# Kernel optimization log

Hardware: AMD Instinct MI355X
Metric: run time of the kernel (lower is better)

## Reference

```python
import jax, jax.numpy as jnp
import numpy as np
import math

D, H, FF, B, S = 512, 8, 2048, 2, 2048
DK = D // H


def _ln(x, g, b, eps=1e-5):
    m = jnp.mean(x, axis=-1, keepdims=True)
    v = jnp.var(x, axis=-1, keepdims=True)
    return (x - m) / jnp.sqrt(v + eps) * g + b


def _mha(q_in, kv_in, Wq, bq, Wk, bk, Wv, bv, Wo, bo):
    Bq, Sq, _ = q_in.shape
    Sk = kv_in.shape[1]
    q = (q_in @ Wq + bq).reshape(Bq, Sq, H, DK).transpose(0, 2, 1, 3)
    k = (kv_in @ Wk + bk).reshape(Bq, Sk, H, DK).transpose(0, 2, 1, 3)
    v = (kv_in @ Wv + bv).reshape(Bq, Sk, H, DK).transpose(0, 2, 1, 3)
    # NOTE: source uses float floor-division `//` by sqrt(dk); replicate faithfully.
    scores = jnp.floor(jnp.einsum('bhqd,bhkd->bhqk', q, k) / math.sqrt(DK))
    # NOTE: source calls scores.masked_fill(...) without assigning -> mask has no effect.
    attn = jax.nn.softmax(scores, axis=-1)
    out = jnp.einsum('bhqk,bhkd->bhqd', attn, v)
    out = out.transpose(0, 2, 1, 3).reshape(Bq, Sq, D)
    return out @ Wo + bo


def setup_inputs() -> dict:
    key = jax.random.key(0)
    ks = jax.random.split(key, 16)
    w = lambda k, shp: jax.random.normal(k, shp, jnp.float32) * 0.02
    inp = {
        'x': jax.random.normal(ks[0], (B, S, D), jnp.float32),
        'enc_out': jax.random.normal(ks[1], (B, S, D), jnp.float32),
        'src_mask': jnp.ones((B, 1, 1, S), jnp.int32),
        'tgt_mask': jnp.ones((B, 1, S, S), jnp.int32),
    }
    for i, pre in enumerate(['sa', 'ca']):
        kk = jax.random.split(ks[2 + i], 4)
        for j, nm in enumerate(['Wq', 'Wk', 'Wv', 'Wo']):
            inp[f'{pre}_{nm}'] = w(kk[j], (D, D))
            inp[f'{pre}_{nm[1].lower()}b'] = jnp.zeros((D,), jnp.float32)
    inp['ff_W1'] = w(ks[4], (D, FF)); inp['ff_b1'] = jnp.zeros((FF,), jnp.float32)
    inp['ff_W2'] = w(ks[5], (FF, D)); inp['ff_b2'] = jnp.zeros((D,), jnp.float32)
    for i in range(3):
        inp[f'ln{i}_g'] = jnp.ones((D,), jnp.float32)
        inp[f'ln{i}_b'] = jnp.zeros((D,), jnp.float32)
    return inp


def reference(x, enc_out, src_mask, tgt_mask,
              sa_Wq, sa_qb, sa_Wk, sa_kb, sa_Wv, sa_vb, sa_Wo, sa_ob,
              ca_Wq, ca_qb, ca_Wk, ca_kb, ca_Wv, ca_vb, ca_Wo, ca_ob,
              ff_W1, ff_b1, ff_W2, ff_b2,
              ln0_g, ln0_b, ln1_g, ln1_b, ln2_g, ln2_b):
    x = _ln(x + _mha(x, x, sa_Wq, sa_qb, sa_Wk, sa_kb, sa_Wv, sa_vb, sa_Wo, sa_ob), ln0_g, ln0_b)
    x = _ln(x + _mha(x, enc_out, ca_Wq, ca_qb, ca_Wk, ca_kb, ca_Wv, ca_vb, ca_Wo, ca_ob), ln1_g, ln1_b)
    ff = jax.nn.relu(x @ ff_W1 + ff_b1) @ ff_W2 + ff_b2
    x = _ln(x + ff, ln2_g, ln2_b)
    return x
```

## Files before the change

### kernel.cpp

```cpp
#include <hip/hip_runtime.h>
#include <math.h>


typedef __attribute__((ext_vector_type(8))) short short8;
typedef __attribute__((ext_vector_type(4))) float f32x4;

#define MFMA16(a, b, c) __builtin_amdgcn_mfma_f32_16x16x32_bf16((a), (b), (c), 0, 0, 0)

__device__ __forceinline__ unsigned short f2bf(float f) {
    unsigned int u = __float_as_uint(f);
    u += 0x7fffu + ((u >> 16) & 1u);
    return (unsigned short)(u >> 16);
}
__device__ __forceinline__ float bf2f(unsigned short h) {
    return __uint_as_float(((unsigned int)h) << 16);
}
__device__ __forceinline__ void g2l16(const void* g, void* l) {
    __builtin_amdgcn_global_load_lds(
        (const __attribute__((address_space(1))) unsigned int*)g,
        (__attribute__((address_space(3))) unsigned int*)l, 16, 0, 0);
}
__device__ __forceinline__ int swz(int row, int col) {
    return row * 64 + (col ^ ((row & 7) * 8));
}
__device__ __forceinline__ void xcd_remap(int& bx, int& by, int& bz) {
    const int gx = gridDim.x, gy = gridDim.y;
    const int nwg = gx * gy * gridDim.z;
    const int flat = blockIdx.x + gx * (blockIdx.y + gy * blockIdx.z);
    const int s = (flat & 7) * (nwg >> 3) + (flat >> 3);
    bx = s % gx; const int t = s / gx; by = t % gy; bz = t / gy;
}

template <int BM, int BN, int MODE>
__global__ __launch_bounds__(256, (BM == 64) ? 4 : (BN == 128 ? 2 : 3))
void gemm_bf16(
    const unsigned short* __restrict__ A, const unsigned short* __restrict__ Bt,
    const float* __restrict__ bias, float* __restrict__ Cf,
    unsigned short* __restrict__ O1,
    int M, int N, int K)
{
    __shared__ unsigned short As[2][BM * 64];
    __shared__ unsigned short Bs[2][BN * 64];
    const int tid = threadIdx.x, wv = tid >> 6, lane = tid & 63;
    const int l15 = lane & 15, l4 = lane >> 4;
    int bx, by, bz; xcd_remap(bx, by, bz);
    const int bm = by * BM, bn = bx * BN;
    constexpr int MI = (BM == 64) ? 1 : (BN == 128 ? 4 : 2);
    constexpr int AJ = (BM == 64) ? 2 : 4;
    constexpr int BJ = (BN == 128) ? 4 : 2;
    const int wrow = (BM == 64) ? wv * 16 : (BN == 128 ? (wv >> 1) * 64 : wv * 32);
    const int wcol = (BN == 128) ? (wv & 1) * 64 : 0;
    const int aw = (BM == 64) ? wv * 16 : wv * 32;
    const int bw = (BN == 128) ? wv * 32 : wv * 16;

    f32x4 acc[MI][4];
    #pragma unroll
    for (int i = 0; i < MI; ++i)
        #pragma unroll
        for (int j = 0; j < 4; ++j) acc[i][j] = (f32x4){0.f, 0.f, 0.f, 0.f};

    const int srow = lane >> 3;
    const int sch  = (lane & 7) ^ srow;
    const unsigned short* Asrc = A + (size_t)(bm + aw + srow) * K + sch * 8;
    const unsigned short* Bsrc = Bt + (size_t)(bn + bw + srow) * K + sch * 8;

    auto stage = [&](int buf, int k0) {
        #pragma unroll
        for (int j = 0; j < AJ; ++j)
            g2l16(Asrc + (size_t)j * 8 * K + k0, &As[buf][(aw + j * 8) * 64]);
        #pragma unroll
        for (int j = 0; j < BJ; ++j)
            g2l16(Bsrc + (size_t)j * 8 * K + k0, &Bs[buf][(bw + j * 8) * 64]);
    };

    stage(0, 0);
    __syncthreads();
    int cur = 0;
    for (int k0 = 0; k0 < K; k0 += 64) {
        if (k0 + 64 < K) stage(cur ^ 1, k0 + 64);
        #pragma unroll
        for (int kk = 0; kk < 2; ++kk) {
            const int kc = kk * 32 + l4 * 8;
            short8 af[MI], bfr[4];
            #pragma unroll
            for (int mi = 0; mi < MI; ++mi)
                af[mi] = *(const short8*)&As[cur][swz(wrow + mi * 16 + l15, kc)];
            #pragma unroll
            for (int nf = 0; nf < 4; ++nf)
                bfr[nf] = *(const short8*)&Bs[cur][swz(wcol + nf * 16 + l15, kc)];
            __builtin_amdgcn_s_setprio(1);
            #pragma unroll
            for (int mi = 0; mi < MI; ++mi)
                #pragma unroll
                for (int nf = 0; nf < 4; ++nf)
                    acc[mi][nf] = MFMA16(af[mi], bfr[nf], acc[mi][nf]);
            __builtin_amdgcn_s_setprio(0);
        }
        __syncthreads();
        cur ^= 1;
    }

    #pragma unroll
    for (int nf = 0; nf < 4; ++nf) {
        const int n = bn + wcol + nf * 16 + l15;
        const float bv = bias[n];
        #pragma unroll
        for (int mi = 0; mi < MI; ++mi) {
            const int m0 = bm + wrow + mi * 16 + l4 * 4;
            #pragma unroll
            for (int r = 0; r < 4; ++r) {
                float v = acc[mi][nf][r] + bv;
                size_t idx = (size_t)(m0 + r) * N + n;
                if (MODE == 0) Cf[idx] = v;
                else           O1[idx] = f2bf(fmaxf(v, 0.f));
            }
        }
    }
}

struct QKVArgs {
    const unsigned short* A[3];
    const unsigned short* Bt[3];
    const float* bias[3];
    unsigned short* O1[3];
    int mode[3];
};
__global__ __launch_bounds__(256, 3) void qkv_gemm(QKVArgs ja)
{
    __shared__ unsigned short As[2][128 * 64];
    __shared__ unsigned short Bs[2][64 * 64];
    const int tid = threadIdx.x, wv = tid >> 6, lane = tid & 63;
    const int l15 = lane & 15, l4 = lane >> 4;
    int bx, by, bz; xcd_remap(bx, by, bz);
    const int bm = by * 128, bn = bx * 64;
    const unsigned short* A  = ja.A[bz];
    const unsigned short* Bt = ja.Bt[bz];
    const int mode = ja.mode[bz];

    f32x4 acc[2][4];
    #pragma unroll
    for (int i = 0; i < 2; ++i)
        #pragma unroll
        for (int j = 0; j < 4; ++j) acc[i][j] = (f32x4){0.f, 0.f, 0.f, 0.f};

    const int srow = lane >> 3, sch = (lane & 7) ^ srow;
    const unsigned short* Asrc = A + (size_t)(bm + wv * 32 + srow) * 512 + sch * 8;
    const unsigned short* Bsrc = Bt + (size_t)(bn + wv * 16 + srow) * 512 + sch * 8;

    auto stage = [&](int buf, int k0) {
        #pragma unroll
        for (int j = 0; j < 4; ++j)
            g2l16(Asrc + (size_t)j * 8 * 512 + k0, &As[buf][(wv * 32 + j * 8) * 64]);
        #pragma unroll
        for (int j = 0; j < 2; ++j)
            g2l16(Bsrc + (size_t)j * 8 * 512 + k0, &Bs[buf][(wv * 16 + j * 8) * 64]);
    };

    stage(0, 0);
    __syncthreads();
    int cur = 0;
    for (int k0 = 0; k0 < 512; k0 += 64) {
        if (k0 + 64 < 512) stage(cur ^ 1, k0 + 64);
        #pragma unroll
        for (int kk = 0; kk < 2; ++kk) {
            const int kc = kk * 32 + l4 * 8;
            short8 af[2], bfr[4];
            af[0] = *(const short8*)&As[cur][swz(wv * 32 + l15, kc)];
            af[1] = *(const short8*)&As[cur][swz(wv * 32 + 16 + l15, kc)];
            #pragma unroll
            for (int nf = 0; nf < 4; ++nf)
                bfr[nf] = *(const short8*)&Bs[cur][swz(nf * 16 + l15, kc)];
            __builtin_amdgcn_s_setprio(1);
            #pragma unroll
            for (int mi = 0; mi < 2; ++mi)
                #pragma unroll
                for (int nf = 0; nf < 4; ++nf)
                    acc[mi][nf] = MFMA16(af[mi], bfr[nf], acc[mi][nf]);
            __builtin_amdgcn_s_setprio(0);
        }
        __syncthreads();
        cur ^= 1;
    }

    #pragma unroll
    for (int nf = 0; nf < 4; ++nf) {
        const int n = bn + nf * 16 + l15;
        const float bv = ja.bias[bz][n];
        #pragma unroll
        for (int mi = 0; mi < 2; ++mi) {
            const int m0 = bm + wv * 32 + mi * 16 + l4 * 4;
            if (mode == 2) {
                ushort4 pk;
                pk.x = f2bf(acc[mi][nf][0] + bv);
                pk.y = f2bf(acc[mi][nf][1] + bv);
                pk.z = f2bf(acc[mi][nf][2] + bv);
                pk.w = f2bf(acc[mi][nf][3] + bv);
                const int hh = n >> 6, dd = n & 63, bb = m0 >> 11, key = m0 & 2047;
                *(ushort4*)(ja.O1[bz] + ((((size_t)bb * 8 + hh) * 64 + dd) * 2048 + key)) = pk;
            } else {
                #pragma unroll
                for (int r = 0; r < 4; ++r)
                    ja.O1[bz][(size_t)(m0 + r) * 512 + n] = f2bf(acc[mi][nf][r] + bv);
            }
        }
    }
}

__global__ __launch_bounds__(256, 2) void attn_mfma(
    const unsigned short* __restrict__ Qb, const unsigned short* __restrict__ Kb,
    const unsigned short* __restrict__ Vt,
    float* __restrict__ PO0, float* __restrict__ PO1, float* __restrict__ PL)
{
    __shared__ unsigned short KH[2][64 * 64];
    __shared__ unsigned short VT[2][64 * 64];
    __shared__ unsigned short PS[64 * 64];

    const int tid = threadIdx.x, wv = tid >> 6, lane = tid & 63;
    const int l15 = lane & 15, l4 = lane >> 4;
    int bx, by, bz; xcd_remap(bx, by, bz);
    const int bh = by, b = bh >> 3, h = bh & 7;
    const int q0 = bx * 64;
    const int srow = lane >> 3;
    const int sch  = (lane & 7) ^ srow;
    const int kt0 = bz * 16, kt1 = kt0 + 16;

    short8 qh[2];
    {
        const size_t qrow = (size_t)(b * 2048 + q0 + wv * 16 + l15) * 512 + h * 64;
        qh[0] = *(const short8*)(Qb + qrow + l4 * 8);
        qh[1] = *(const short8*)(Qb + qrow + 32 + l4 * 8);
    }

    const unsigned short* k_src  = Kb + (size_t)(b * 2048 + wv * 16 + srow) * 512 + h * 64 + sch * 8;
    const unsigned short* vt_src = Vt + (size_t)(bh * 64 + wv * 16 + srow) * 2048 + sch * 8;

    auto stageKV = [&](int buf, int kt) {
        const size_t k0 = (size_t)kt * 64;
        #pragma unroll
        for (int j = 0; j < 2; ++j) {
            g2l16(k_src + (k0 + j * 8) * 512, &KH[buf][(wv * 16 + j * 8) * 64]);
            g2l16(vt_src + k0 + (size_t)j * 8 * 2048, &VT[buf][(wv * 16 + j * 8) * 64]);
        }
    };

    f32x4 o[4], lacc;
    #pragma unroll
    for (int i = 0; i < 4; ++i) o[i] = (f32x4){0.f, 0.f, 0.f, 0.f};
    lacc = (f32x4){0.f, 0.f, 0.f, 0.f};

    const short one_s = (short)(l15 == 0 ? 0x3F80 : 0);
    const short8 oneb = {one_s, one_s, one_s, one_s, one_s, one_s, one_s, one_s};

    stageKV(0, kt0);
    __syncthreads();
    int cur = 0;
    for (int kt = kt0; kt < kt1; ++kt) {
        if (kt + 1 < kt1) stageKV(cur ^ 1, kt + 1);

        f32x4 s[4];
        __builtin_amdgcn_s_setprio(1);
        #pragma unroll
        for (int f = 0; f < 4; ++f) {
            s[f] = (f32x4){0.f, 0.f, 0.f, 0.f};
            #pragma unroll
            for (int kk = 0; kk < 2; ++kk) {
                short8 kbf = *(const short8*)&KH[cur][swz(f * 16 + l15, kk * 32 + l4 * 8)];
                s[f] = MFMA16(qh[kk], kbf, s[f]);
            }
        }
        __builtin_amdgcn_s_setprio(0);

        #pragma unroll
        for (int f = 0; f < 4; ++f)
            #pragma unroll
            for (int r = 0; r < 4; ++r)
                PS[swz(wv * 16 + l4 * 4 + r, f * 16 + l15)] =
                    f2bf(__expf(floorf(s[f][r] * 0.125f)));

        short8 pa[2];
        pa[0] = *(const short8*)&PS[swz(wv * 16 + l15, l4 * 8)];
        pa[1] = *(const short8*)&PS[swz(wv * 16 + l15, 32 + l4 * 8)];

        __builtin_amdgcn_s_setprio(1);
        lacc = MFMA16(pa[0], oneb, lacc);
        lacc = MFMA16(pa[1], oneb, lacc);
        #pragma unroll
        for (int df = 0; df < 4; ++df) {
            #pragma unroll
            for (int kk = 0; kk < 2; ++kk) {
                short8 vb = *(const short8*)&VT[cur][swz(df * 16 + l15, kk * 32 + l4 * 8)];
                o[df] = MFMA16(pa[kk], vb, o[df]);
            }
        }
        __builtin_amdgcn_s_setprio(0);
        __syncthreads();
        cur ^= 1;
    }

    float* PO = bz ? PO1 : PO0;
    #pragma unroll
    for (int df = 0; df < 4; ++df)
        #pragma unroll
        for (int r = 0; r < 4; ++r)
            PO[(size_t)(b * 2048 + q0 + wv * 16 + l4 * 4 + r) * 512 + h * 64 + df * 16 + l15]
                = o[df][r];
    if (l15 == 0) {
        #pragma unroll
        for (int r = 0; r < 4; ++r)
            PL[(bz * 16 + bh) * 2048 + q0 + wv * 16 + l4 * 4 + r] = lacc[r];
    }
}

__global__ __launch_bounds__(256) void attn_combine(
    const float* __restrict__ po0, const float* __restrict__ po1,
    const float* __restrict__ pl, unsigned short* __restrict__ Ob)
{
    const size_t i = ((size_t)blockIdx.x * 256 + threadIdx.x) * 8;
    const int row = (int)(i >> 9), col = (int)(i & 511);
    const int b = row >> 11, q = row & 2047, h = col >> 6;
    const int bh = b * 8 + h;
    const float inv = 1.f / (pl[bh * 2048 + q] + pl[(16 + bh) * 2048 + q]);
    float4 a0 = *(const float4*)(po0 + i), a1 = *(const float4*)(po0 + i + 4);
    float4 c0 = *(const float4*)(po1 + i), c1 = *(const float4*)(po1 + i + 4);
    uint4 u;
    u.x = (unsigned)f2bf((a0.x + c0.x) * inv) | ((unsigned)f2bf((a0.y + c0.y) * inv) << 16);
    u.y = (unsigned)f2bf((a0.z + c0.z) * inv) | ((unsigned)f2bf((a0.w + c0.w) * inv) << 16);
    u.z = (unsigned)f2bf((a1.x + c1.x) * inv) | ((unsigned)f2bf((a1.y + c1.y) * inv) << 16);
    u.w = (unsigned)f2bf((a1.z + c1.z) * inv) | ((unsigned)f2bf((a1.w + c1.w) * inv) << 16);
    *(uint4*)(Ob + i) = u;
}

template <bool XBF, bool OUTF, bool OUTB>
__global__ __launch_bounds__(256) void add_ln(
    const void* __restrict__ Xv, const float* __restrict__ R,
    const float* __restrict__ g, const float* __restrict__ beta,
    float* __restrict__ OutF, unsigned short* __restrict__ OutB)
{
    const int row = blockIdx.x * 4 + (threadIdx.x >> 6);
    const int lane = threadIdx.x & 63;
    const int c0 = lane * 8;
    float v[8];
    const float* rr = R + (size_t)row * 512 + c0;
    float4 r0 = *(const float4*)rr, r1 = *(const float4*)(rr + 4);
    float xx[8];
    if (XBF) {
        const unsigned short* xr = (const unsigned short*)Xv + (size_t)row * 512 + c0;
        uint4 u = *(const uint4*)xr;
        xx[0] = bf2f(u.x & 0xffff); xx[1] = bf2f(u.x >> 16);
        xx[2] = bf2f(u.y & 0xffff); xx[3] = bf2f(u.y >> 16);
        xx[4] = bf2f(u.z & 0xffff); xx[5] = bf2f(u.z >> 16);
        xx[6] = bf2f(u.w & 0xffff); xx[7] = bf2f(u.w >> 16);
    } else {
        const float* xr = (const float*)Xv + (size_t)row * 512 + c0;
        float4 a0 = *(const float4*)xr, a1 = *(const float4*)(xr + 4);
        xx[0] = a0.x; xx[1] = a0.y; xx[2] = a0.z; xx[3] = a0.w;
        xx[4] = a1.x; xx[5] = a1.y; xx[6] = a1.z; xx[7] = a1.w;
    }
    v[0] = xx[0] + r0.x; v[1] = xx[1] + r0.y; v[2] = xx[2] + r0.z; v[3] = xx[3] + r0.w;
    v[4] = xx[4] + r1.x; v[5] = xx[5] + r1.y; v[6] = xx[6] + r1.z; v[7] = xx[7] + r1.w;
    float s = 0.f, s2 = 0.f;
    #pragma unroll
    for (int j = 0; j < 8; ++j) { s += v[j]; s2 += v[j] * v[j]; }
    #pragma unroll
    for (int off = 1; off < 64; off <<= 1) {
        s  += __shfl_xor(s, off);
        s2 += __shfl_xor(s2, off);
    }
    const float mean = s * (1.f / 512.f);
    const float var = s2 * (1.f / 512.f) - mean * mean;
    const float rs = 1.f / sqrtf(var + 1e-5f);
    float ovals[8];
    const float* gg = g + c0; const float* bb = beta + c0;
    #pragma unroll
    for (int j = 0; j < 8; ++j) ovals[j] = (v[j] - mean) * rs * gg[j] + bb[j];
    if (OUTF) {
        float* po = OutF + (size_t)row * 512 + c0;
        *(float4*)po = (float4){ovals[0], ovals[1], ovals[2], ovals[3]};
        *(float4*)(po + 4) = (float4){ovals[4], ovals[5], ovals[6], ovals[7]};
    }
    if (OUTB) {
        uint4 u;
        u.x = (unsigned)f2bf(ovals[0]) | ((unsigned)f2bf(ovals[1]) << 16);
        u.y = (unsigned)f2bf(ovals[2]) | ((unsigned)f2bf(ovals[3]) << 16);
        u.z = (unsigned)f2bf(ovals[4]) | ((unsigned)f2bf(ovals[5]) << 16);
        u.w = (unsigned)f2bf(ovals[6]) | ((unsigned)f2bf(ovals[7]) << 16);
        *(uint4*)(OutB + (size_t)row * 512 + c0) = u;
    }
}

struct WTJobs {
    const float* src[10];
    unsigned short* dst[10];
    int K[10], N[10];
    int cum[11];
};
__global__ __launch_bounds__(256) void prep(
    const float* __restrict__ X, const float* __restrict__ E,
    unsigned short* __restrict__ Xb, unsigned short* __restrict__ Eb, WTJobs jb)
{
    __shared__ float T[32][33];
    const int bid = blockIdx.x;
    if (bid < 2048) {
        size_t i = ((size_t)bid * 256 + threadIdx.x) * 8;
        const float* src; unsigned short* dst; size_t off;
        if (i < 2097152) { src = X; dst = Xb; off = i; }
        else             { src = E; dst = Eb; off = i - 2097152; }
        float4 a = *(const float4*)(src + off), c = *(const float4*)(src + off + 4);
        uint4 u;
        u.x = (unsigned)f2bf(a.x) | ((unsigned)f2bf(a.y) << 16);
        u.y = (unsigned)f2bf(a.z) | ((unsigned)f2bf(a.w) << 16);
        u.z = (unsigned)f2bf(c.x) | ((unsigned)f2bf(c.y) << 16);
        u.w = (unsigned)f2bf(c.z) | ((unsigned)f2bf(c.w) << 16);
        *(uint4*)(dst + off) = u;
        return;
    }
    int wb = bid - 2048;
    int z = 0;
    while (wb >= jb.cum[z + 1]) ++z;
    const int lt = wb - jb.cum[z];
    const int K = jb.K[z], N = jb.N[z];
    const int ntx = N >> 5;
    const int tx = lt % ntx, ty = lt / ntx;
    const int r = threadIdx.x >> 3, c4 = (threadIdx.x & 7) * 4;
    float4 a = *(const float4*)(jb.src[z] + (size_t)(ty * 32 + r) * N + tx * 32 + c4);
    T[r][c4] = a.x; T[r][c4 + 1] = a.y; T[r][c4 + 2] = a.z; T[r][c4 + 3] = a.w;
    __syncthreads();
    ushort4 o;
    o.x = f2bf(T[c4][r]); o.y = f2bf(T[c4 + 1][r]);
    o.z = f2bf(T[c4 + 2][r]); o.w = f2bf(T[c4 + 3][r]);
    *(ushort4*)(jb.dst[z] + (size_t)(tx * 32 + r) * K + ty * 32 + c4) = o;
}

extern "C" void kernel_launch(void* const* d_in, const int* in_sizes, int n_in,
                              void* d_out, int out_size, void* d_ws, size_t ws_size,
                              hipStream_t stream)
{
    const float* x   = (const float*)d_in[0];
    const float* enc = (const float*)d_in[1];
    const float* Wp[8] = {(const float*)d_in[4],  (const float*)d_in[6],
                          (const float*)d_in[8],  (const float*)d_in[10],
                          (const float*)d_in[12], (const float*)d_in[14],
                          (const float*)d_in[16], (const float*)d_in[18]};
    const float* sa_qb = (const float*)d_in[5],  *sa_kb = (const float*)d_in[7];
    const float* sa_vb = (const float*)d_in[9],  *sa_ob = (const float*)d_in[11];
    const float* ca_qb = (const float*)d_in[13], *ca_kb = (const float*)d_in[15];
    const float* ca_vb = (const float*)d_in[17], *ca_ob = (const float*)d_in[19];
    const float* ff_W1 = (const float*)d_in[20], *ff_b1 = (const float*)d_in[21];
    const float* ff_W2 = (const float*)d_in[22], *ff_b2 = (const float*)d_in[23];
    const float* ln0_g = (const float*)d_in[24], *ln0_b = (const float*)d_in[25];
    const float* ln1_g = (const float*)d_in[26], *ln1_b = (const float*)d_in[27];
    const float* ln2_g = (const float*)d_in[28], *ln2_b = (const float*)d_in[29];

    char* base = (char*)d_ws;
    const size_t MB = 1u << 20;
    unsigned short* wt   = (unsigned short*)(base + 0 * MB);
    unsigned short* xb   = (unsigned short*)(base + 8 * MB);
    unsigned short* encb = (unsigned short*)(base + 12 * MB);
    unsigned short* x1b  = (unsigned short*)(base + 16 * MB);
    unsigned short* attnb= (unsigned short*)(base + 20 * MB);
    unsigned short* vt   = (unsigned short*)(base + 24 * MB);
    unsigned short* qb   = (unsigned short*)(base + 28 * MB);
    unsigned short* kb   = (unsigned short*)(base + 32 * MB);
    unsigned short* ffb  = qb;
    unsigned short* x2b  = xb;
    float* proj = (float*)(base + 44 * MB);
    float* pl   = (float*)(base + 52 * MB);
    float* po0  = proj;
    float* po1  = (float*)d_out;
    float* out  = (float*)d_out;

    unsigned short* wtp[10];
    for (int i = 0; i < 8; ++i) wtp[i] = wt + (size_t)i * 262144;
    wtp[8] = wt + 8u * 262144;
    wtp[9] = wt + 8u * 262144 + 1048576;

    WTJobs jb;
    for (int i = 0; i < 8; ++i) { jb.src[i] = Wp[i]; jb.dst[i] = wtp[i]; jb.K[i] = 512; jb.N[i] = 512; }
    jb.src[8] = ff_W1; jb.dst[8] = wtp[8]; jb.K[8] = 512;  jb.N[8] = 2048;
    jb.src[9] = ff_W2; jb.dst[9] = wtp[9]; jb.K[9] = 2048; jb.N[9] = 512;
    jb.cum[0] = 0;
    for (int i = 0; i < 10; ++i)
        jb.cum[i + 1] = jb.cum[i] + (jb.N[i] >> 5) * (jb.K[i] >> 5);

    QKVArgs sa, ca;
    sa.A[0] = xb;  sa.Bt[0] = wtp[0]; sa.bias[0] = sa_qb; sa.O1[0] = qb; sa.mode[0] = 4;
    sa.A[1] = xb;  sa.Bt[1] = wtp[1]; sa.bias[1] = sa_kb; sa.O1[1] = kb; sa.mode[1] = 4;
    sa.A[2] = xb;  sa.Bt[2] = wtp[2]; sa.bias[2] = sa_vb; sa.O1[2] = vt; sa.mode[2] = 2;
    ca.A[0] = x1b;  ca.Bt[0] = wtp[4]; ca.bias[0] = ca_qb; ca.O1[0] = qb; ca.mode[0] = 4;
    ca.A[1] = encb; ca.Bt[1] = wtp[5]; ca.bias[1] = ca_kb; ca.O1[1] = kb; ca.mode[1] = 4;
    ca.A[2] = encb; ca.Bt[2] = wtp[6]; ca.bias[2] = ca_vb; ca.O1[2] = vt; ca.mode[2] = 2;

    dim3 blk(256);
    dim3 gqkv(8, 32, 3);
    dim3 g64(8, 64);
    dim3 gff1(16, 32);
    dim3 gattn(32, 16, 2);
    dim3 gln(1024);

    prep<<<2048 + jb.cum[10], blk, 0, stream>>>(x, enc, xb, encb, jb);

    qkv_gemm<<<gqkv, blk, 0, stream>>>(sa);
    attn_mfma<<<gattn, blk, 0, stream>>>(qb, kb, vt, po0, po1, pl);
    attn_combine<<<1024, blk, 0, stream>>>(po0, po1, pl, attnb);
    gemm_bf16<64, 64, 0><<<g64, blk, 0, stream>>>(attnb, wtp[3], sa_ob, proj, nullptr, 4096, 512, 512);
    add_ln<false, false, true><<<gln, blk, 0, stream>>>(x, proj, ln0_g, ln0_b, nullptr, x1b);

    qkv_gemm<<<gqkv, blk, 0, stream>>>(ca);
    attn_mfma<<<gattn, blk, 0, stream>>>(qb, kb, vt, po0, po1, pl);
    attn_combine<<<1024, blk, 0, stream>>>(po0, po1, pl, attnb);
    gemm_bf16<64, 64, 0><<<g64, blk, 0, stream>>>(attnb, wtp[7], ca_ob, proj, nullptr, 4096, 512, 512);
    add_ln<true, false, true><<<gln, blk, 0, stream>>>(x1b, proj, ln1_g, ln1_b, nullptr, x2b);

    gemm_bf16<128, 128, 3><<<gff1, blk, 0, stream>>>(x2b, wtp[8], ff_b1, nullptr, ffb, 4096, 2048, 512);
    gemm_bf16<64, 64, 0><<<g64, blk, 0, stream>>>(ffb, wtp[9], ff_b2, proj, nullptr, 4096, 512, 2048);
    add_ln<true, true, false><<<gln, blk, 0, stream>>>(x2b, proj, ln2_g, ln2_b, out, nullptr);
}
```

Before: 186.5 us.

## Store projection outputs in bf16 and permute P/V layout for packed stores

The output-projection and FF2 GEMMs now write bf16 instead of fp32, and add_ln gains a template flag to read a bf16 residual. This halves the traffic for the projection buffer on three write/read round-trips, at the cost of rounding the pre-LayerNorm residual to bf16. In attention, the P tile is now written with packed v_cvt_pk_bf16_f32 and 8-byte stores instead of scalar 2-byte stores. The V-transpose layout is permuted within 64-key blocks to match the new P column order. The V-transpose write in the QKV GEMM now uses strided scalar stores instead of a ushort4 store.

```diff
diff --git a/kernel.cpp b/kernel.cpp
--- a/kernel.cpp
+++ b/kernel.cpp
@@ -111,8 +111,9 @@
             for (int r = 0; r < 4; ++r) {
                 float v = acc[mi][nf][r] + bv;
                 size_t idx = (size_t)(m0 + r) * N + n;
-                if (MODE == 0) Cf[idx] = v;
-                else           O1[idx] = f2bf(fmaxf(v, 0.f));
+                if (MODE == 0)      Cf[idx] = v;
+                else if (MODE == 3) O1[idx] = f2bf(fmaxf(v, 0.f));
+                else                O1[idx] = f2bf(v);
             }
         }
     }
@@ -190,13 +191,14 @@
         for (int mi = 0; mi < 2; ++mi) {
             const int m0 = bm + wv * 32 + mi * 16 + l4 * 4;
             if (mode == 2) {
-                ushort4 pk;
-                pk.x = f2bf(acc[mi][nf][0] + bv);
-                pk.y = f2bf(acc[mi][nf][1] + bv);
-                pk.z = f2bf(acc[mi][nf][2] + bv);
-                pk.w = f2bf(acc[mi][nf][3] + bv);
-                const int hh = n >> 6, dd = n & 63, bb = m0 >> 11, key = m0 & 2047;
-                *(ushort4*)(ja.O1[bz] + ((((size_t)bb * 8 + hh) * 64 + dd) * 2048 + key)) = pk;
+                const int hh = n >> 6, dd = n & 63, bb = m0 >> 11;
+                const int key = m0 & 2047;
+                const int f = (key & 63) >> 4, j0 = key & 15;
+                const size_t basevt = (((size_t)bb * 8 + hh) * 64 + dd) * 2048
+                                    + (key & ~63) + f;
+                #pragma unroll
+                for (int r = 0; r < 4; ++r)
+                    ja.O1[bz][basevt + (size_t)(j0 + r) * 4] = f2bf(acc[mi][nf][r] + bv);
             } else {
                 #pragma unroll
                 for (int r = 0; r < 4; ++r)
@@ -271,11 +273,16 @@
         __builtin_amdgcn_s_setprio(0);
 
         #pragma unroll
-        for (int f = 0; f < 4; ++f)
-            #pragma unroll
-            for (int r = 0; r < 4; ++r)
-                PS[swz(wv * 16 + l4 * 4 + r, f * 16 + l15)] =
-                    f2bf(__expf(floorf(s[f][r] * 0.125f)));
+        for (int r = 0; r < 4; ++r) {
+            float p0 = __expf(floorf(s[0][r] * 0.125f));
+            float p1 = __expf(floorf(s[1][r] * 0.125f));
+            float p2 = __expf(floorf(s[2][r] * 0.125f));
+            float p3 = __expf(floorf(s[3][r] * 0.125f));
+            unsigned u0, u1;
+            asm("v_cvt_pk_bf16_f32 %0, %1, %2" : "=v"(u0) : "v"(p0), "v"(p1));
+            asm("v_cvt_pk_bf16_f32 %0, %1, %2" : "=v"(u1) : "v"(p2), "v"(p3));
+            *(uint2*)&PS[swz(wv * 16 + l4 * 4 + r, l15 * 4)] = (uint2){u0, u1};
+        }
 
         short8 pa[2];
         pa[0] = *(const short8*)&PS[swz(wv * 16 + l15, l4 * 8)];
@@ -330,19 +337,16 @@
     *(uint4*)(Ob + i) = u;
 }
 
-template <bool XBF, bool OUTF, bool OUTB>
+template <bool XBF, bool RBF, bool OUTF, bool OUTB>
 __global__ __launch_bounds__(256) void add_ln(
-    const void* __restrict__ Xv, const float* __restrict__ R,
+    const void* __restrict__ Xv, const void* __restrict__ Rv,
     const float* __restrict__ g, const float* __restrict__ beta,
     float* __restrict__ OutF, unsigned short* __restrict__ OutB)
 {
     const int row = blockIdx.x * 4 + (threadIdx.x >> 6);
     const int lane = threadIdx.x & 63;
     const int c0 = lane * 8;
-    float v[8];
-    const float* rr = R + (size_t)row * 512 + c0;
-    float4 r0 = *(const float4*)rr, r1 = *(const float4*)(rr + 4);
-    float xx[8];
+    float xx[8], rr[8], v[8];
     if (XBF) {
         const unsigned short* xr = (const unsigned short*)Xv + (size_t)row * 512 + c0;
         uint4 u = *(const uint4*)xr;
@@ -356,11 +360,25 @@
         xx[0] = a0.x; xx[1] = a0.y; xx[2] = a0.z; xx[3] = a0.w;
         xx[4] = a1.x; xx[5] = a1.y; xx[6] = a1.z; xx[7] = a1.w;
     }
-    v[0] = xx[0] + r0.x; v[1] = xx[1] + r0.y; v[2] = xx[2] + r0.z; v[3] = xx[3] + r0.w;
-    v[4] = xx[4] + r1.x; v[5] = xx[5] + r1.y; v[6] = xx[6] + r1.z; v[7] = xx[7] + r1.w;
+    if (RBF) {
+        const unsigned short* xr = (const unsigned short*)Rv + (size_t)row * 512 + c0;
+        uint4 u = *(const uint4*)xr;
+        rr[0] = bf2f(u.x & 0xffff); rr[1] = bf2f(u.x >> 16);
+        rr[2] = bf2f(u.y & 0xffff); rr[3] = bf2f(u.y >> 16);
+        rr[4] = bf2f(u.z & 0xffff); rr[5] = bf2f(u.z >> 16);
+        rr[6] = bf2f(u.w & 0xffff); rr[7] = bf2f(u.w >> 16);
+    } else {
+        const float* xr = (const float*)Rv + (size_t)row * 512 + c0;
+        float4 a0 = *(const float4*)xr, a1 = *(const float4*)(xr + 4);
+        rr[0] = a0.x; rr[1] = a0.y; rr[2] = a0.z; rr[3] = a0.w;
+        rr[4] = a1.x; rr[5] = a1.y; rr[6] = a1.z; rr[7] = a1.w;
+    }
     float s = 0.f, s2 = 0.f;
     #pragma unroll
-    for (int j = 0; j < 8; ++j) { s += v[j]; s2 += v[j] * v[j]; }
+    for (int j = 0; j < 8; ++j) {
+        v[j] = xx[j] + rr[j];
+        s += v[j]; s2 += v[j] * v[j];
+    }
     #pragma unroll
     for (int off = 1; off < 64; off <<= 1) {
         s  += __shfl_xor(s, off);
@@ -453,21 +471,21 @@
 
     char* base = (char*)d_ws;
     const size_t MB = 1u << 20;
-    unsigned short* wt   = (unsigned short*)(base + 0 * MB);
-    unsigned short* xb   = (unsigned short*)(base + 8 * MB);
-    unsigned short* encb = (unsigned short*)(base + 12 * MB);
-    unsigned short* x1b  = (unsigned short*)(base + 16 * MB);
-    unsigned short* attnb= (unsigned short*)(base + 20 * MB);
-    unsigned short* vt   = (unsigned short*)(base + 24 * MB);
-    unsigned short* qb   = (unsigned short*)(base + 28 * MB);
-    unsigned short* kb   = (unsigned short*)(base + 32 * MB);
-    unsigned short* ffb  = qb;
-    unsigned short* x2b  = xb;
-    float* proj = (float*)(base + 44 * MB);
-    float* pl   = (float*)(base + 52 * MB);
-    float* po0  = proj;
-    float* po1  = (float*)d_out;
-    float* out  = (float*)d_out;
+    unsigned short* wt    = (unsigned short*)(base + 0 * MB);
+    unsigned short* xb    = (unsigned short*)(base + 8 * MB);
+    unsigned short* encb  = (unsigned short*)(base + 12 * MB);
+    unsigned short* x1b   = (unsigned short*)(base + 16 * MB);
+    unsigned short* attnb = (unsigned short*)(base + 20 * MB);
+    unsigned short* vt    = (unsigned short*)(base + 24 * MB);
+    unsigned short* qb    = (unsigned short*)(base + 28 * MB);
+    unsigned short* kb    = (unsigned short*)(base + 32 * MB);
+    float*          pl    = (float*)(base + 36 * MB);
+    unsigned short* projb = (unsigned short*)(base + 44 * MB);
+    float*          po0   = (float*)(base + 48 * MB);
+    unsigned short* ffb   = qb;
+    unsigned short* x2b   = xb;
+    float* po1 = (float*)d_out;
+    float* out = (float*)d_out;
 
     unsigned short* wtp[10];
     for (int i = 0; i < 8; ++i) wtp[i] = wt + (size_t)i * 262144;
@@ -502,16 +520,16 @@
     qkv_gemm<<<gqkv, blk, 0, stream>>>(sa);
     attn_mfma<<<gattn, blk, 0, stream>>>(qb, kb, vt, po0, po1, pl);
     attn_combine<<<1024, blk, 0, stream>>>(po0, po1, pl, attnb);
-    gemm_bf16<64, 64, 0><<<g64, blk, 0, stream>>>(attnb, wtp[3], sa_ob, proj, nullptr, 4096, 512, 512);
-    add_ln<false, false, true><<<gln, blk, 0, stream>>>(x, proj, ln0_g, ln0_b, nullptr, x1b);
+    gemm_bf16<64, 64, 4><<<g64, blk, 0, stream>>>(attnb, wtp[3], sa_ob, nullptr, projb, 4096, 512, 512);
+    add_ln<false, true, false, true><<<gln, blk, 0, stream>>>(x, projb, ln0_g, ln0_b, nullptr, x1b);
 
     qkv_gemm<<<gqkv, blk, 0, stream>>>(ca);
     attn_mfma<<<gattn, blk, 0, stream>>>(qb, kb, vt, po0, po1, pl);
     attn_combine<<<1024, blk, 0, stream>>>(po0, po1, pl, attnb);
-    gemm_bf16<64, 64, 0><<<g64, blk, 0, stream>>>(attnb, wtp[7], ca_ob, proj, nullptr, 4096, 512, 512);
-    add_ln<true, false, true><<<gln, blk, 0, stream>>>(x1b, proj, ln1_g, ln1_b, nullptr, x2b);
+    gemm_bf16<64, 64, 4><<<g64, blk, 0, stream>>>(attnb, wtp[7], ca_ob, nullptr, projb, 4096, 512, 512);
+    add_ln<true, true, false, true><<<gln, blk, 0, stream>>>(x1b, projb, ln1_g, ln1_b, nullptr, x2b);
 
     gemm_bf16<128, 128, 3><<<gff1, blk, 0, stream>>>(x2b, wtp[8], ff_b1, nullptr, ffb, 4096, 2048, 512);
-    gemm_bf16<64, 64, 0><<<g64, blk, 0, stream>>>(ffb, wtp[9], ff_b2, proj, nullptr, 4096, 512, 2048);
-    add_ln<true, true, false><<<gln, blk, 0, stream>>>(x2b, proj, ln2_g, ln2_b, out, nullptr);
-}
+    gemm_bf16<64, 64, 4><<<g64, blk, 0, stream>>>(ffb, wtp[9], ff_b2, nullptr, projb, 4096, 512, 2048);
+    add_ln<true, true, true, false><<<gln, blk, 0, stream>>>(x2b, projb, ln2_g, ln2_b, out, nullptr);
+}
```

Result: slower. 193.0 us (+3.5%).
